# Optimization experiments

Hardware: AMD Instinct MI355X
Metric: run time of the kernel (lower is better)

## Reference

```python
import jax, jax.numpy as jnp
import numpy as np

B, D, K, P = 512, 2048, 128, 5

def setup_inputs() -> dict:
    key = jax.random.key(0)
    k1, k2 = jax.random.split(key)
    x = jax.random.normal(k1, (B, D), dtype=jnp.float32)
    theta = 0.05 * jax.random.normal(k2, (D, K, P), dtype=jnp.float32)
    log_weight_scale = jnp.zeros((K, P), dtype=jnp.float32)
    bias = -jnp.ones((K,), dtype=jnp.float32)  # layer inits bias to -1
    return {"x": x, "theta": theta, "log_weight_scale": log_weight_scale, "bias": bias}

def reference(x, theta, log_weight_scale, bias):
    b = x.shape[0]
    # weight-normalized kernel: [D, K, P]
    norm = jnp.sqrt(jnp.sum(theta * theta, axis=0))            # [K, P]
    kernel = theta * (jnp.exp(log_weight_scale) / norm)[None]  # [D, K, P]
    actv = jnp.einsum('bd,dkp->bkp', x, kernel)                # [B, K, P]
    # pairwise L1 over P: [B, K, B]
    diff = jnp.abs(actv[:, :, :, None] - jnp.transpose(actv, (1, 2, 0))[None])  # [B,K,P,B]
    abs_dif = jnp.sum(diff, axis=2) + 1e6 * jnp.eye(b, dtype=x.dtype)[:, None, :]
    f = jnp.sum(jnp.exp(-abs_dif), axis=2) + bias[None, :]     # [B, K]
    return jnp.concatenate([x, f], axis=1)                     # [B, D+K]
```

## Files before the change

kernel.cpp:

```cpp
#include <hip/hip_runtime.h>
#include <math.h>

#define BSZ 512
#define DD 2048
#define KK 128
#define PP 5
#define NCOL (KK * PP)
#define OUTW (DD + KK)
#define LOG2E 1.4426950408889634f

#define KSPLIT 16
#define GK (DD / KSPLIT)
#define QSPLIT 8

typedef __attribute__((ext_vector_type(8))) short bf16x8;
typedef __attribute__((ext_vector_type(4))) float f32x4;

#define WS_NORM 0
#define WS_ACTV (WS_NORM + NCOL)
#define WS_FPART (WS_ACTV + BSZ * NCOL)
#define WS_XB (WS_FPART + QSPLIT * KK * BSZ)
#define WS_THT (WS_XB + BSZ * DD / 2)
#define WS_PART (WS_THT + NCOL * DD / 2)

__device__ inline ushort f2b(float f) {
    unsigned u = __float_as_uint(f);
    u += 0x7FFF + ((u >> 16) & 1);
    return (ushort)(u >> 16);
}

#define SWZ(r, c) ((((r) * 128) + ((c) ^ (((r) & 7) << 3))))

__global__ __launch_bounds__(256) void prep_kernel(const float* __restrict__ theta,
                                                   const float* __restrict__ x,
                                                   float* __restrict__ norm,
                                                   ushort* __restrict__ thT,
                                                   ushort* __restrict__ xb) {
    __shared__ float partial[32][8];
    __shared__ ushort sT[64][68];

    const int bid = blockIdx.x;
    const int t   = threadIdx.x;

    if (bid < 80) {
        const int c8  = bid * 8;
        const int col = c8 + (t & 7);
        const int g   = t >> 3;
        const float* p = theta + (size_t)g * NCOL + col;
        float s = 0.f;
#pragma unroll
        for (int j = 0; j < 64; ++j) {
            float v = p[(size_t)j * 32 * NCOL];
            s += v * v;
        }
        partial[g][t & 7] = s;
        __syncthreads();
        if (t < 8) {
            float acc = 0.f;
#pragma unroll
            for (int gg = 0; gg < 32; ++gg) acc += partial[gg][t];
            norm[c8 + t] = acc;
        }
    } else if (bid < 400) {
        const int tb    = bid - 80;
        const int kz    = (tb & 31) * 64;
        const int nz    = (tb >> 5) * 64;
        const int c4    = t & 15;
        const int rbase = t >> 4;
#pragma unroll
        for (int i = 0; i < 4; ++i) {
            int r = rbase + i * 16;
            float4 v = *(const float4*)&theta[(size_t)(kz + r) * NCOL + nz + c4 * 4];
            sT[c4 * 4 + 0][r] = f2b(v.x);
            sT[c4 * 4 + 1][r] = f2b(v.y);
            sT[c4 * 4 + 2][r] = f2b(v.z);
            sT[c4 * 4 + 3][r] = f2b(v.w);
        }
        __syncthreads();
#pragma unroll
        for (int i = 0; i < 2; ++i) {
            int slot = t + i * 256;
            int rr   = slot >> 3;
            int cc   = (slot & 7) * 8;
            ushort4 w0 = *(const ushort4*)&sT[rr][cc];
            ushort4 w1 = *(const ushort4*)&sT[rr][cc + 4];
            ushort* dst = &thT[(size_t)(nz + rr) * DD + kz + cc];
            *(ushort4*)&dst[0] = w0;
            *(ushort4*)&dst[4] = w1;
        }
    } else {
        const int b2 = bid - 400;
#pragma unroll
        for (int i = 0; i < 4; ++i) {
            int base = b2 * 4096 + i * 1024 + t * 4;
            float4 v = *(const float4*)&x[base];
            ushort4 w;
            w.x = f2b(v.x); w.y = f2b(v.y); w.z = f2b(v.z); w.w = f2b(v.w);
            *(ushort4*)&xb[base] = w;
        }
    }
}

__global__ __launch_bounds__(256) void gemm_kernel(const ushort* __restrict__ xb,
                                                   const ushort* __restrict__ thT,
                                                   float* __restrict__ part,
                                                   const float* __restrict__ x,
                                                   float* __restrict__ out) {
    __shared__ ushort lA[64 * 128];
    __shared__ ushort lB[64 * 128];

    const int bx = blockIdx.x;
    if (bx >= 1280) {
        const int bid = bx - 1280;
        for (int i = bid * 256 + threadIdx.x; i < BSZ * (DD / 4); i += 80 * 256) {
            int r = i >> 9;
            int c = i & 511;
            float4 v = *(const float4*)&x[(size_t)r * DD + c * 4];
            *(float4*)&out[(size_t)r * OUTW + c * 4] = v;
        }
        return;
    }

    const int t    = threadIdx.x;
    const int lane = t & 63;
    const int wave = t >> 6;
    const int tile = bx % 80;
    const int z    = bx / 80;
    const int bn   = (tile % 10) * 64;
    const int bm   = (tile / 10) * 64;
    const int kz   = z * GK;

    const ushort* gA = xb  + (size_t)bm * DD + kz;
    const ushort* gB = thT + (size_t)bn * DD + kz;

    const int srr = t >> 4;
    const int sss = t & 15;

    uint4 va[4], vb[4];
#pragma unroll
    for (int i = 0; i < 4; ++i) {
        int rr = srr + i * 16;
        va[i] = *(const uint4*)&gA[(size_t)rr * DD + sss * 8];
        vb[i] = *(const uint4*)&gB[(size_t)rr * DD + sss * 8];
    }
#pragma unroll
    for (int i = 0; i < 4; ++i) {
        int rr = srr + i * 16;
        *(uint4*)&lA[SWZ(rr, sss * 8)] = va[i];
        *(uint4*)&lB[SWZ(rr, sss * 8)] = vb[i];
    }
    __syncthreads();

    const int fr = lane & 15;
    const int g  = lane >> 4;
    const int mr = (wave >> 1) * 32 + fr;
    const int nr = (wave & 1) * 32 + fr;

    f32x4 acc[2][2] = {};
#pragma unroll
    for (int ks = 0; ks < 4; ++ks) {
        const int kc = ks * 32 + g * 8;
        bf16x8 a0 = *(const bf16x8*)&lA[SWZ(mr,      kc)];
        bf16x8 a1 = *(const bf16x8*)&lA[SWZ(mr + 16, kc)];
        bf16x8 b0 = *(const bf16x8*)&lB[SWZ(nr,      kc)];
        bf16x8 b1 = *(const bf16x8*)&lB[SWZ(nr + 16, kc)];
        acc[0][0] = __builtin_amdgcn_mfma_f32_16x16x32_bf16(a0, b0, acc[0][0], 0, 0, 0);
        acc[0][1] = __builtin_amdgcn_mfma_f32_16x16x32_bf16(a0, b1, acc[0][1], 0, 0, 0);
        acc[1][0] = __builtin_amdgcn_mfma_f32_16x16x32_bf16(a1, b0, acc[1][0], 0, 0, 0);
        acc[1][1] = __builtin_amdgcn_mfma_f32_16x16x32_bf16(a1, b1, acc[1][1], 0, 0, 0);
    }

    float* base = part + (size_t)z * (BSZ * NCOL);
#pragma unroll
    for (int mt = 0; mt < 2; ++mt)
#pragma unroll
        for (int nt = 0; nt < 2; ++nt) {
            int row = bm + (wave >> 1) * 32 + mt * 16 + g * 4;
            int col = bn + (wave & 1) * 32 + nt * 16 + fr;
            float* dst = base + (size_t)row * NCOL + col;
#pragma unroll
            for (int reg = 0; reg < 4; ++reg)
                dst[(size_t)reg * NCOL] = acc[mt][nt][reg];
        }
}

__global__ __launch_bounds__(256) void reduce_kernel(const float* __restrict__ part,
                                                     const float* __restrict__ norm,
                                                     const float* __restrict__ lws,
                                                     float* __restrict__ actv) {
    int i   = blockIdx.x * 256 + threadIdx.x;
    int col = i % NCOL;
    float s = 0.f;
#pragma unroll
    for (int q = 0; q < KSPLIT; ++q)
        s += part[(size_t)q * (BSZ * NCOL) + i];
    const float scale = __builtin_amdgcn_exp2f(lws[col] * LOG2E) *
                        __builtin_amdgcn_rsqf(norm[col]) * LOG2E;
    actv[i] = s * scale;
}

__global__ __launch_bounds__(256) void pairwise_kernel(const float* __restrict__ actv,
                                                       float* __restrict__ f_part) {
    const int k   = blockIdx.x;
    const int q   = blockIdx.y;
    const int tid = threadIdx.x;

    __shared__ float sB[64][8];

    for (int i = tid; i < 64 * PP; i += 256) {
        int r = i / PP;
        int p = i - r * PP;
        sB[r][p] = actv[(size_t)(q * 64 + r) * NCOL + k * PP + p];
    }

    float a[2][PP];
#pragma unroll
    for (int r = 0; r < 2; ++r) {
        const float* ap = &actv[(size_t)(tid + r * 256) * NCOL + k * PP];
#pragma unroll
        for (int p = 0; p < PP; ++p) a[r][p] = ap[p];
    }
    __syncthreads();

    float acc[2] = {0.f, 0.f};
#pragma unroll 4
    for (int j = 0; j < 64; ++j) {
        const float4 v  = *(const float4*)&sB[j][0];
        const float  v4 = sB[j][4];
#pragma unroll
        for (int r = 0; r < 2; ++r) {
            float s = fabsf(a[r][0] - v.x) + fabsf(a[r][1] - v.y) +
                      fabsf(a[r][2] - v.z) + fabsf(a[r][3] - v.w) +
                      fabsf(a[r][4] - v4);
            acc[r] += __builtin_amdgcn_exp2f(-s);
        }
    }

    float* fp = f_part + ((size_t)q * KK + k) * BSZ;
    fp[tid]       = acc[0];
    fp[tid + 256] = acc[1];
}

__global__ __launch_bounds__(256) void freduce_kernel(const float* __restrict__ f_part,
                                                      const float* __restrict__ bias,
                                                      float* __restrict__ out) {
    int i = blockIdx.x * 256 + threadIdx.x;
    int k = i >> 9;
    int b = i & 511;
    float s = 0.f;
#pragma unroll
    for (int q = 0; q < QSPLIT; ++q)
        s += f_part[((size_t)q * KK + k) * BSZ + b];
    out[(size_t)b * OUTW + DD + k] = s - 1.0f + bias[k];
}

extern "C" void kernel_launch(void* const* d_in, const int* in_sizes, int n_in,
                              void* d_out, int out_size, void* d_ws, size_t ws_size,
                              hipStream_t stream) {
    const float* x     = (const float*)d_in[0];
    const float* theta = (const float*)d_in[1];
    const float* lws   = (const float*)d_in[2];
    const float* bias  = (const float*)d_in[3];
    float* out = (float*)d_out;

    float* ws     = (float*)d_ws;
    float* norm   = ws + WS_NORM;
    float* actv   = ws + WS_ACTV;
    float* f_part = ws + WS_FPART;
    ushort* xb    = (ushort*)(ws + WS_XB);
    ushort* thT   = (ushort*)(ws + WS_THT);
    float* part   = ws + WS_PART;

    prep_kernel<<<656, 256, 0, stream>>>(theta, x, norm, thT, xb);
    gemm_kernel<<<1360, 256, 0, stream>>>(xb, thT, part, x, out);
    reduce_kernel<<<(BSZ * NCOL) / 256, 256, 0, stream>>>(part, norm, lws, actv);
    pairwise_kernel<<<dim3(KK, QSPLIT), 256, 0, stream>>>(actv, f_part);
    freduce_kernel<<<256, 256, 0, stream>>>(f_part, bias, out);
}
```

Baseline: 104.0 us.

## Fuse reduce, pairwise and final reduce into one cooperative kernel; bf16 GEMM partials

Merges the split-K reduction, the pairwise L1/exp kernel and the final f reduction into one cooperative kernel that uses grid.sync between phases, saving two launches. GEMM split-K partials are now written as bf16 instead of fp32, halving partial traffic at some cost in accuracy. The GEMM block index mapping is also reordered so that neighbouring blocks share the same N tile. Grid-wide syncs add their own cost, and the cooperative launch of 1024 blocks requires that many blocks be resident at once.

Result: slower. 269.5 us (+159.1%).

```diff
diff --git a/kernel.cpp b/kernel.cpp
--- a/kernel.cpp
+++ b/kernel.cpp
@@ -1,5 +1,8 @@
 #include <hip/hip_runtime.h>
+#include <hip/hip_cooperative_groups.h>
 #include <math.h>
+
+namespace cg = cooperative_groups;
 
 #define BSZ 512
 #define DD 2048
@@ -27,6 +30,9 @@
     unsigned u = __float_as_uint(f);
     u += 0x7FFF + ((u >> 16) & 1);
     return (ushort)(u >> 16);
+}
+__device__ inline float b2f(ushort h) {
+    return __uint_as_float((unsigned)h << 16);
 }
 
 #define SWZ(r, c) ((((r) * 128) + ((c) ^ (((r) & 7) << 3))))
@@ -103,7 +109,7 @@
 
 __global__ __launch_bounds__(256) void gemm_kernel(const ushort* __restrict__ xb,
                                                    const ushort* __restrict__ thT,
-                                                   float* __restrict__ part,
+                                                   ushort* __restrict__ parth,
                                                    const float* __restrict__ x,
                                                    float* __restrict__ out) {
     __shared__ ushort lA[64 * 128];
@@ -124,10 +130,11 @@
     const int t    = threadIdx.x;
     const int lane = t & 63;
     const int wave = t >> 6;
-    const int tile = bx % 80;
-    const int z    = bx / 80;
-    const int bn   = (tile % 10) * 64;
-    const int bm   = (tile / 10) * 64;
+    const int mt8  = bx & 7;
+    const int rest = bx >> 3;
+    const int bn   = (rest % 10) * 64;
+    const int bm   = mt8 * 64;
+    const int z    = rest / 10;
     const int kz   = z * GK;
 
     const ushort* gA = xb  + (size_t)bm * DD + kz;
@@ -170,88 +177,103 @@
         acc[1][1] = __builtin_amdgcn_mfma_f32_16x16x32_bf16(a1, b1, acc[1][1], 0, 0, 0);
     }
 
-    float* base = part + (size_t)z * (BSZ * NCOL);
+    ushort* base = parth + (size_t)z * (BSZ * NCOL);
 #pragma unroll
     for (int mt = 0; mt < 2; ++mt)
 #pragma unroll
         for (int nt = 0; nt < 2; ++nt) {
             int row = bm + (wave >> 1) * 32 + mt * 16 + g * 4;
             int col = bn + (wave & 1) * 32 + nt * 16 + fr;
-            float* dst = base + (size_t)row * NCOL + col;
+            ushort* dst = base + (size_t)row * NCOL + col;
 #pragma unroll
             for (int reg = 0; reg < 4; ++reg)
-                dst[(size_t)reg * NCOL] = acc[mt][nt][reg];
-        }
-}
-
-__global__ __launch_bounds__(256) void reduce_kernel(const float* __restrict__ part,
-                                                     const float* __restrict__ norm,
-                                                     const float* __restrict__ lws,
-                                                     float* __restrict__ actv) {
-    int i   = blockIdx.x * 256 + threadIdx.x;
-    int col = i % NCOL;
-    float s = 0.f;
-#pragma unroll
-    for (int q = 0; q < KSPLIT; ++q)
-        s += part[(size_t)q * (BSZ * NCOL) + i];
-    const float scale = __builtin_amdgcn_exp2f(lws[col] * LOG2E) *
-                        __builtin_amdgcn_rsqf(norm[col]) * LOG2E;
-    actv[i] = s * scale;
-}
-
-__global__ __launch_bounds__(256) void pairwise_kernel(const float* __restrict__ actv,
-                                                       float* __restrict__ f_part) {
-    const int k   = blockIdx.x;
-    const int q   = blockIdx.y;
+                dst[(size_t)reg * NCOL] = f2b(acc[mt][nt][reg]);
+        }
+}
+
+__global__ __launch_bounds__(256, 4) void fused_kernel(const ushort* __restrict__ parth,
+                                                       const float* __restrict__ norm,
+                                                       const float* __restrict__ lws,
+                                                       float* __restrict__ actv,
+                                                       float* __restrict__ f_part,
+                                                       const float* __restrict__ bias,
+                                                       float* __restrict__ out) {
+    cg::grid_group grid = cg::this_grid();
     const int tid = threadIdx.x;
+    const int bid = blockIdx.x;
 
     __shared__ float sB[64][8];
 
-    for (int i = tid; i < 64 * PP; i += 256) {
-        int r = i / PP;
-        int p = i - r * PP;
-        sB[r][p] = actv[(size_t)(q * 64 + r) * NCOL + k * PP + p];
-    }
-
-    float a[2][PP];
-#pragma unroll
-    for (int r = 0; r < 2; ++r) {
-        const float* ap = &actv[(size_t)(tid + r * 256) * NCOL + k * PP];
-#pragma unroll
-        for (int p = 0; p < PP; ++p) a[r][p] = ap[p];
-    }
-    __syncthreads();
-
-    float acc[2] = {0.f, 0.f};
+    {
+        int i = bid * 256 + tid;
+#pragma unroll
+        for (int rep = 0; rep < 2; ++rep) {
+            if (i < BSZ * NCOL) {
+                int col = i % NCOL;
+                float s = 0.f;
+#pragma unroll
+                for (int q = 0; q < KSPLIT; ++q)
+                    s += b2f(parth[(size_t)q * (BSZ * NCOL) + i]);
+                const float scale = __builtin_amdgcn_exp2f(lws[col] * LOG2E) *
+                                    __builtin_amdgcn_rsqf(norm[col]) * LOG2E;
+                actv[i] = s * scale;
+            }
+            i += 1024 * 256;
+        }
+    }
+    grid.sync();
+
+    {
+        const int k = bid & 127;
+        const int q = bid >> 7;
+
+        for (int i = tid; i < 64 * PP; i += 256) {
+            int r = i / PP;
+            int p = i - r * PP;
+            sB[r][p] = actv[(size_t)(q * 64 + r) * NCOL + k * PP + p];
+        }
+
+        float a[2][PP];
+#pragma unroll
+        for (int r = 0; r < 2; ++r) {
+            const float* ap = &actv[(size_t)(tid + r * 256) * NCOL + k * PP];
+#pragma unroll
+            for (int p = 0; p < PP; ++p) a[r][p] = ap[p];
+        }
+        __syncthreads();
+
+        float acc[2] = {0.f, 0.f};
 #pragma unroll 4
-    for (int j = 0; j < 64; ++j) {
-        const float4 v  = *(const float4*)&sB[j][0];
-        const float  v4 = sB[j][4];
-#pragma unroll
-        for (int r = 0; r < 2; ++r) {
-            float s = fabsf(a[r][0] - v.x) + fabsf(a[r][1] - v.y) +
-                      fabsf(a[r][2] - v.z) + fabsf(a[r][3] - v.w) +
-                      fabsf(a[r][4] - v4);
-            acc[r] += __builtin_amdgcn_exp2f(-s);
-        }
-    }
-
-    float* fp = f_part + ((size_t)q * KK + k) * BSZ;
-    fp[tid]       = acc[0];
-    fp[tid + 256] = acc[1];
-}
-
-__global__ __launch_bounds__(256) void freduce_kernel(const float* __restrict__ f_part,
-                                                      const float* __restrict__ bias,
-                                                      float* __restrict__ out) {
-    int i = blockIdx.x * 256 + threadIdx.x;
-    int k = i >> 9;
-    int b = i & 511;
-    float s = 0.f;
-#pragma unroll
-    for (int q = 0; q < QSPLIT; ++q)
-        s += f_part[((size_t)q * KK + k) * BSZ + b];
-    out[(size_t)b * OUTW + DD + k] = s - 1.0f + bias[k];
+        for (int j = 0; j < 64; ++j) {
+            const float4 v  = *(const float4*)&sB[j][0];
+            const float  v4 = sB[j][4];
+#pragma unroll
+            for (int r = 0; r < 2; ++r) {
+                float s = fabsf(a[r][0] - v.x) + fabsf(a[r][1] - v.y) +
+                          fabsf(a[r][2] - v.z) + fabsf(a[r][3] - v.w) +
+                          fabsf(a[r][4] - v4);
+                acc[r] += __builtin_amdgcn_exp2f(-s);
+            }
+        }
+
+        float* fp = f_part + ((size_t)q * KK + k) * BSZ;
+        fp[tid]       = acc[0];
+        fp[tid + 256] = acc[1];
+    }
+    grid.sync();
+
+    {
+        int i = bid * 256 + tid;
+        if (i < BSZ * KK) {
+            int k = i >> 9;
+            int b = i & 511;
+            float s = 0.f;
+#pragma unroll
+            for (int q = 0; q < QSPLIT; ++q)
+                s += f_part[((size_t)q * KK + k) * BSZ + b];
+            out[(size_t)b * OUTW + DD + k] = s - 1.0f + bias[k];
+        }
+    }
 }
 
 extern "C" void kernel_launch(void* const* d_in, const int* in_sizes, int n_in,
@@ -269,11 +291,14 @@
     float* f_part = ws + WS_FPART;
     ushort* xb    = (ushort*)(ws + WS_XB);
     ushort* thT   = (ushort*)(ws + WS_THT);
-    float* part   = ws + WS_PART;
+    ushort* parth = (ushort*)(ws + WS_PART);
 
     prep_kernel<<<656, 256, 0, stream>>>(theta, x, norm, thT, xb);
-    gemm_kernel<<<1360, 256, 0, stream>>>(xb, thT, part, x, out);
-    reduce_kernel<<<(BSZ * NCOL) / 256, 256, 0, stream>>>(part, norm, lws, actv);
-    pairwise_kernel<<<dim3(KK, QSPLIT), 256, 0, stream>>>(actv, f_part);
-    freduce_kernel<<<256, 256, 0, stream>>>(f_part, bias, out);
-}
+    gemm_kernel<<<1360, 256, 0, stream>>>(xb, thT, parth, x, out);
+
+    const ushort* parth_c = parth;
+    void* args[] = { (void*)&parth_c, (void*)&norm, (void*)&lws, (void*)&actv,
+                     (void*)&f_part, (void*)&bias, (void*)&out };
+    hipLaunchCooperativeKernel((void*)fused_kernel, dim3(1024), dim3(256),
+                               args, 0, stream);
+}
```
